# Optimization experiments

Measured on AMD Instinct MI355X. Metric: run time of the kernel, lower is better.

The kernel has to match this reference:

```python
import jax, jax.numpy as jnp
import numpy as np

B, N, D, H = 4, 2048, 512, 8
HD = D // H
SCALE = D ** (-0.5)  # module uses embed_dim**-0.5, not head_dim**-0.5


def setup_inputs() -> dict:
    key = jax.random.key(0)
    k1, k2, k3, k4 = jax.random.split(key, 4)
    x = jax.random.normal(k1, (B, N, D), dtype=jnp.float32)
    # qkv: Linear(D, 3D, bias=False); store as [D, 3D] (x @ W_qkv)
    w_qkv = jax.random.normal(k2, (D, 3 * D), dtype=jnp.float32) * (D ** -0.5)
    # out_proj: Linear(D, D) with bias
    w_out = jax.random.normal(k3, (D, D), dtype=jnp.float32) * (D ** -0.5)
    b_out = jax.random.normal(k4, (D,), dtype=jnp.float32) * 0.01
    return {"x": x, "w_qkv": w_qkv, "w_out": w_out, "b_out": b_out}


def reference(x, w_qkv, w_out, b_out):
    # qkv projection -> [B, N, 3, H, HD] -> split
    qkv = (x @ w_qkv).reshape(B, N, 3, H, HD)
    q = qkv[:, :, 0].transpose(0, 2, 1, 3)  # [B, H, N, HD]
    k = qkv[:, :, 1].transpose(0, 2, 1, 3)
    v = qkv[:, :, 2].transpose(0, 2, 1, 3)
    attn = jnp.einsum("bhqd,bhkd->bhqk", q, k) * SCALE  # [B, H, N, N]
    attn = jax.nn.softmax(attn, axis=-1)
    out = jnp.einsum("bhqk,bhkd->bhqd", attn, v)  # [B, H, N, HD]
    out = out.transpose(0, 2, 1, 3).reshape(B, N, D)
    return out @ w_out + b_out
```

## Files before the change

kernel.cpp:

```cpp
#include <hip/hip_runtime.h>

typedef __attribute__((ext_vector_type(4))) float f32x4;
typedef __attribute__((ext_vector_type(16))) float f32x16;
typedef __attribute__((ext_vector_type(8))) short short8;

#define DEV static __device__ __forceinline__

DEV unsigned short f2bf(float f) {
  union { float f; unsigned u; } x; x.f = f;
  unsigned r = x.u + 0x7fffu + ((x.u >> 16) & 1u);
  return (unsigned short)(r >> 16);
}

DEV float bf2f(unsigned short u) {
  union { unsigned u; float f; } x; x.u = ((unsigned)u) << 16;
  return x.f;
}

DEV f32x4 mfma16(short8 a, short8 b, f32x4 c) {
  return __builtin_amdgcn_mfma_f32_16x16x32_bf16(a, b, c, 0, 0, 0);
}

DEV f32x16 mfma32(short8 a, short8 b, f32x16 c) {
  return __builtin_amdgcn_mfma_f32_32x32x16_bf16(a, b, c, 0, 0, 0);
}

DEV void gload16(const void* g, void* l) {
  __builtin_amdgcn_global_load_lds(
      (const __attribute__((address_space(1))) void*)g,
      (__attribute__((address_space(3))) void*)l, 16, 0, 0);
}

DEV float exp2f_fast(float x) {
  float r;
  asm("v_exp_f32 %0, %1" : "=v"(r) : "v"(x));
  return r;
}

DEV unsigned cvtpk(float lo, float hi) {
  unsigned r;
  asm("v_cvt_pk_bf16_f32 %0, %1, %2" : "=v"(r) : "v"(lo), "v"(hi));
  return r;
}

DEV short8 mk8(unsigned w0, unsigned w1, unsigned w2, unsigned w3) {
  union { unsigned u[4]; short8 s; } x;
  x.u[0] = w0; x.u[1] = w1; x.u[2] = w2; x.u[3] = w3;
  return x.s;
}

__global__ __launch_bounds__(256) void k_convert(const float* __restrict__ in,
                                                 unsigned short* __restrict__ out) {
  size_t i = (size_t)blockIdx.x * 256 + threadIdx.x;
  const f32x4* p = (const f32x4*)(in + i * 8);
  f32x4 a = p[0], b = p[1];
  short8 r;
  r[0] = f2bf(a[0]); r[1] = f2bf(a[1]); r[2] = f2bf(a[2]); r[3] = f2bf(a[3]);
  r[4] = f2bf(b[0]); r[5] = f2bf(b[1]); r[6] = f2bf(b[2]); r[7] = f2bf(b[3]);
  *(short8*)(out + i * 8) = r;
}

__global__ __launch_bounds__(256) void k_transpose_f32_bf16(
    const float* __restrict__ in, unsigned short* __restrict__ out, int R, int C) {
  __shared__ unsigned short T[64 * 72];
  int r0 = blockIdx.y * 64, c0 = blockIdx.x * 64;
  int t = threadIdx.x;
  int rr = t >> 2, seg = t & 3;
  const float* p = in + (size_t)(r0 + rr) * C + c0 + seg * 16;
#pragma unroll
  for (int q = 0; q < 4; ++q) {
    f32x4 v = *(const f32x4*)(p + q * 4);
#pragma unroll
    for (int e = 0; e < 4; ++e) T[rr * 72 + seg * 16 + q * 4 + e] = f2bf(v[e]);
  }
  __syncthreads();
  short8 o0, o1;
#pragma unroll
  for (int e = 0; e < 8; ++e) o0[e] = (short)T[(seg * 16 + e) * 72 + rr];
#pragma unroll
  for (int e = 0; e < 8; ++e) o1[e] = (short)T[(seg * 16 + 8 + e) * 72 + rr];
  unsigned short* q2 = out + (size_t)(c0 + rr) * R + r0 + seg * 16;
  *(short8*)q2 = o0;
  *(short8*)(q2 + 8) = o1;
}

__global__ __launch_bounds__(256) void k_build_vt(const unsigned short* __restrict__ qkv,
                                                  unsigned short* __restrict__ vt) {
  __shared__ unsigned short T[64 * 72];
  int n0 = blockIdx.x * 64;
  int bh = blockIdx.y;
  int b = bh >> 3, h = bh & 7;
  int t = threadIdx.x;
  int rr = t >> 2, seg = t & 3;
  const unsigned short* p =
      qkv + (size_t)(b * 2048 + n0 + rr) * 1536 + 1024 + h * 64 + seg * 16;
  *(short8*)&T[rr * 72 + seg * 16] = *(const short8*)p;
  *(short8*)&T[rr * 72 + seg * 16 + 8] = *(const short8*)(p + 8);
  __syncthreads();
  short8 o0, o1;
#pragma unroll
  for (int e = 0; e < 8; ++e) o0[e] = (short)T[(seg * 16 + e) * 72 + rr];
#pragma unroll
  for (int e = 0; e < 8; ++e) o1[e] = (short)T[(seg * 16 + 8 + e) * 72 + rr];
  unsigned short* q2 = vt + (size_t)(bh * 64 + rr) * 2048 + n0 + seg * 16;
  *(short8*)q2 = o0;
  *(short8*)(q2 + 8) = o1;
}

template <bool F32OUT>
__global__ __launch_bounds__(256) void k_gemm_bt(
    const unsigned short* __restrict__ A, const unsigned short* __restrict__ Bt,
    void* __restrict__ Cp, const float* __restrict__ bias, int M, int N, int K) {
  __shared__ unsigned short Asm[128 * 64];
  __shared__ unsigned short Bsm[128 * 64];
  const int tid = threadIdx.x;
  const int lane = tid & 63, w = tid >> 6;
  const int wr = w >> 1, wc = w & 1;
  const int bm = blockIdx.y * 128, bn = blockIdx.x * 128;
  const int l15 = lane & 15, l4 = lane >> 4;
  f32x4 acc[4][4] = {};
  for (int k0 = 0; k0 < K; k0 += 64) {
    __syncthreads();
#pragma unroll
    for (int j = 0; j < 4; ++j) {
      int c = j * 256 + tid;
      gload16(A + (size_t)(bm + (c >> 3)) * K + k0 + ((c & 7) << 3),
              Asm + (size_t)(j * 256 + w * 64) * 8);
    }
#pragma unroll
    for (int j = 0; j < 4; ++j) {
      int c = j * 256 + tid;
      gload16(Bt + (size_t)(bn + (c >> 3)) * K + k0 + ((c & 7) << 3),
              Bsm + (size_t)(j * 256 + w * 64) * 8);
    }
    __syncthreads();
#pragma unroll
    for (int kc = 0; kc < 2; ++kc) {
      short8 av[4], bv[4];
#pragma unroll
      for (int i = 0; i < 4; ++i)
        av[i] = *(const short8*)&Asm[(wr * 64 + i * 16 + l15) * 64 + kc * 32 + l4 * 8];
#pragma unroll
      for (int j = 0; j < 4; ++j)
        bv[j] = *(const short8*)&Bsm[(wc * 64 + j * 16 + l15) * 64 + kc * 32 + l4 * 8];
#pragma unroll
      for (int i = 0; i < 4; ++i)
#pragma unroll
        for (int j = 0; j < 4; ++j)
          acc[i][j] = mfma16(av[i], bv[j], acc[i][j]);
    }
  }
#pragma unroll
  for (int i = 0; i < 4; ++i) {
#pragma unroll
    for (int j = 0; j < 4; ++j) {
      int col = bn + wc * 64 + j * 16 + l15;
      float bb = 0.f;
      if constexpr (F32OUT) bb = bias[col];
#pragma unroll
      for (int v = 0; v < 4; ++v) {
        int row = bm + wr * 64 + i * 16 + l4 * 4 + v;
        if constexpr (F32OUT) {
          ((float*)Cp)[(size_t)row * N + col] = acc[i][j][v] + bb;
        } else {
          ((unsigned short*)Cp)[(size_t)row * N + col] = f2bf(acc[i][j][v]);
        }
      }
    }
  }
}

__global__ __launch_bounds__(512, 4) void k_attn4(const unsigned short* __restrict__ qkv,
                                                  const unsigned short* __restrict__ vtg,
                                                  unsigned short* __restrict__ O) {
  __shared__ unsigned short smem[16896];
  unsigned short* Ks0 = smem;
  unsigned short* Ks1 = smem + 4096;
  unsigned short* Vs0 = smem + 8192;
  unsigned short* Vs1 = smem + 12288;
  const int tid = threadIdx.x;
  const int lane = tid & 63, w = tid >> 6;
  const int qg = w & 3, half = w >> 2;
  const int l31 = lane & 31, hi = lane >> 5;
  const int bh = blockIdx.y, b = bh >> 3, h = bh & 7;
  const int q0 = blockIdx.x * 128 + qg * 32;
  const float CL = 0.044194173824159216f * 1.4426950408889634f;

  short8 qf[4];
  {
    const unsigned short* qp = qkv + (size_t)(b * 2048 + q0 + l31) * 1536 + h * 64;
#pragma unroll
    for (int ks = 0; ks < 4; ++ks) {
      short8 raw = *(const short8*)(qp + ks * 16 + hi * 8);
      short8 f;
#pragma unroll
      for (int e = 0; e < 8; ++e)
        f[e] = (short)f2bf(bf2f((unsigned short)raw[e]) * CL);
      qf[ks] = f;
    }
  }

  const int sr = tid >> 3, seg = tid & 7;
  const unsigned short* kg = qkv + (size_t)b * 2048 * 1536 + 512 + h * 64 + seg * 8;
  const unsigned short* vg = vtg + (size_t)bh * 64 * 2048 + seg * 8;
  const int so = sr * 64 + ((seg * 8) ^ ((sr & 7) << 3));

  *(short8*)&Ks0[so] = *(const short8*)(kg + (size_t)sr * 1536);
  *(short8*)&Vs0[so] = *(const short8*)(vg + (size_t)sr * 2048);
  __syncthreads();

  const int rsw = (l31 & 7) << 3;
  const int krow = (half * 32 + l31) * 64;

  f32x16 oacc0 = {}, oacc1 = {};
  float m_run = 0.f, l_run = 0.f;
  unsigned short* kcur = Ks0; unsigned short* knxt = Ks1;
  unsigned short* vcur = Vs0; unsigned short* vnxt = Vs1;

  for (int t = 0; t < 32; ++t) {
    short8 pk, pv;
    if (t < 31) {
      int kv = (t + 1) * 64;
      pk = *(const short8*)(kg + (size_t)(kv + sr) * 1536);
      pv = *(const short8*)(vg + (size_t)sr * 2048 + kv);
    }

    f32x16 st = {};
    __builtin_amdgcn_s_setprio(1);
#pragma unroll
    for (int ks = 0; ks < 4; ++ks) {
      int col = ks * 16 + hi * 8;
      short8 kf = *(const short8*)&kcur[krow + (col ^ rsw)];
      st = mfma32(kf, qf[ks], st);
    }
    __builtin_amdgcn_s_setprio(0);

    float tm[8];
#pragma unroll
    for (int r = 0; r < 8; ++r) tm[r] = fmaxf(st[r], st[r + 8]);
    float pm = fmaxf(fmaxf(fmaxf(tm[0], tm[1]), fmaxf(tm[2], tm[3])),
                     fmaxf(fmaxf(tm[4], tm[5]), fmaxf(tm[6], tm[7])));
    pm = fmaxf(pm, __shfl_xor(pm, 32));

    if (!__all(pm <= m_run + 11.5f)) {
      float mn = fmaxf(m_run, pm);
      float al = exp2f_fast(m_run - mn);
#pragma unroll
      for (int r = 0; r < 16; ++r) {
        int qd = (r & 3) + 8 * (r >> 2) + 4 * hi;
        float a = __shfl(al, qd);
        oacc0[r] *= a;
        oacc1[r] *= a;
      }
      l_run *= al;
      m_run = mn;
    }

    float p[16];
    float la = 0.f, lb = 0.f;
#pragma unroll
    for (int r = 0; r < 8; ++r) { p[r] = exp2f_fast(st[r] - m_run); la += p[r]; }
#pragma unroll
    for (int r = 8; r < 16; ++r) { p[r] = exp2f_fast(st[r] - m_run); lb += p[r]; }
    float lsum = la + lb;
    short8 pa[2];
#pragma unroll
    for (int g = 0; g < 2; ++g) {
      unsigned pkA0 = cvtpk(p[8 * g + 0], p[8 * g + 1]);
      unsigned pkA1 = cvtpk(p[8 * g + 2], p[8 * g + 3]);
      unsigned pkB0 = cvtpk(p[8 * g + 4], p[8 * g + 5]);
      unsigned pkB1 = cvtpk(p[8 * g + 6], p[8 * g + 7]);
      unsigned tA0 = __shfl_xor(pkA0, 32), tA1 = __shfl_xor(pkA1, 32);
      unsigned tB0 = __shfl_xor(pkB0, 32), tB1 = __shfl_xor(pkB1, 32);
      unsigned w0 = hi ? tB0 : pkA0;
      unsigned w1 = hi ? tB1 : pkA1;
      unsigned w2 = hi ? pkB0 : tA0;
      unsigned w3 = hi ? pkB1 : tA1;
      pa[g] = mk8(w0, w1, w2, w3);
    }
    lsum += __shfl_xor(lsum, 32);
    l_run += lsum;

    __builtin_amdgcn_s_setprio(1);
#pragma unroll
    for (int ks = 0; ks < 2; ++ks) {
      int col = (half * 2 + ks) * 16 + hi * 8;
      short8 vf0 = *(const short8*)&vcur[l31 * 64 + (col ^ rsw)];
      short8 vf1 = *(const short8*)&vcur[(32 + l31) * 64 + (col ^ rsw)];
      oacc0 = mfma32(pa[ks], vf0, oacc0);
      oacc1 = mfma32(pa[ks], vf1, oacc1);
    }
    __builtin_amdgcn_s_setprio(0);

    if (t < 31) {
      *(short8*)&knxt[so] = pk;
      *(short8*)&vnxt[so] = pv;
    }
    __syncthreads();
    { unsigned short* tp = kcur; kcur = knxt; knxt = tp; }
    { unsigned short* tp = vcur; vcur = vnxt; vnxt = tp; }
  }

  float* Opart = (float*)smem;
  float* mlbuf = (float*)(smem + 16384);
  if (half == 1) {
    float* op = Opart + qg * 2048;
#pragma unroll
    for (int r = 0; r < 16; ++r) {
      int qd = (r & 3) + 8 * (r >> 2) + 4 * hi;
      op[qd * 64 + l31] = oacc0[r];
      op[qd * 64 + 32 + l31] = oacc1[r];
    }
    if (hi == 0) {
      mlbuf[qg * 64 + l31] = m_run;
      mlbuf[qg * 64 + 32 + l31] = l_run;
    }
  }
  __syncthreads();
  if (half == 0) {
    float mb = mlbuf[qg * 64 + l31];
    float lb2 = mlbuf[qg * 64 + 32 + l31];
    float mmax = fmaxf(m_run, mb);
    float sa = exp2f_fast(m_run - mmax);
    float sb = exp2f_fast(mb - mmax);
    float dI = 1.0f / (l_run * sa + lb2 * sb);
    float fA = sa * dI, fB = sb * dI;
    const float* op = Opart + qg * 2048;
#pragma unroll
    for (int r = 0; r < 16; ++r) {
      int qd = (r & 3) + 8 * (r >> 2) + 4 * hi;
      float fa = __shfl(fA, qd), fb = __shfl(fB, qd);
      float o0 = oacc0[r] * fa + op[qd * 64 + l31] * fb;
      float o1 = oacc1[r] * fa + op[qd * 64 + 32 + l31] * fb;
      size_t row = (size_t)(b * 2048 + q0 + qd) * 512 + h * 64;
      O[row + l31] = f2bf(o0);
      O[row + 32 + l31] = f2bf(o1);
    }
  }
}

extern "C" void kernel_launch(void* const* d_in, const int* in_sizes, int n_in,
                              void* d_out, int out_size, void* d_ws, size_t ws_size,
                              hipStream_t stream) {
  const float* x = (const float*)d_in[0];
  const float* w_qkv = (const float*)d_in[1];
  const float* w_out = (const float*)d_in[2];
  const float* b_out = (const float*)d_in[3];
  float* out = (float*)d_out;
  char* ws = (char*)d_ws;

  unsigned short* xb    = (unsigned short*)(ws + 0);
  unsigned short* wqkvT = (unsigned short*)(ws + 8388608);
  unsigned short* woutT = (unsigned short*)(ws + 9961472);
  unsigned short* qkvb  = (unsigned short*)(ws + 10485760);
  unsigned short* vtb   = (unsigned short*)(ws + 35651584);
  unsigned short* Ob    = (unsigned short*)(ws + 44040192);

  k_convert<<<2048, 256, 0, stream>>>(x, xb);
  k_transpose_f32_bf16<<<dim3(24, 8), 256, 0, stream>>>(w_qkv, wqkvT, 512, 1536);
  k_transpose_f32_bf16<<<dim3(8, 8), 256, 0, stream>>>(w_out, woutT, 512, 512);
  k_gemm_bt<false><<<dim3(12, 64), 256, 0, stream>>>(xb, wqkvT, (void*)qkvb, nullptr,
                                                     8192, 1536, 512);
  k_build_vt<<<dim3(32, 32), 256, 0, stream>>>(qkvb, vtb);
  k_attn4<<<dim3(16, 32), 512, 0, stream>>>(qkvb, vtb, Ob);
  k_gemm_bt<true><<<dim3(4, 64), 256, 0, stream>>>(Ob, woutT, (void*)out, b_out,
                                                   8192, 512, 512);
}
```

Measured before the change: 182.0 us.

## Fuse prep kernels, swizzle GEMM block order for XCDs, widen LDS XOR swizzle

Merges the x conversion and both weight transposes into one launch, removing two kernel launches. Remaps GEMM block indices so consecutive blocks are spread across the 8 XCDs, aiming for better L2 locality. Changes the attention LDS swizzle to XOR row bits 0-2 with bits 3-5, which changes the bank mapping for K and V fragment reads and may reduce conflicts. These three ideas are unrelated to one another.

```diff
diff --git a/kernel.cpp b/kernel.cpp
--- a/kernel.cpp
+++ b/kernel.cpp
@@ -49,22 +49,37 @@
   return x.s;
 }
 
-__global__ __launch_bounds__(256) void k_convert(const float* __restrict__ in,
-                                                 unsigned short* __restrict__ out) {
-  size_t i = (size_t)blockIdx.x * 256 + threadIdx.x;
-  const f32x4* p = (const f32x4*)(in + i * 8);
-  f32x4 a = p[0], b = p[1];
-  short8 r;
-  r[0] = f2bf(a[0]); r[1] = f2bf(a[1]); r[2] = f2bf(a[2]); r[3] = f2bf(a[3]);
-  r[4] = f2bf(b[0]); r[5] = f2bf(b[1]); r[6] = f2bf(b[2]); r[7] = f2bf(b[3]);
-  *(short8*)(out + i * 8) = r;
-}
-
-__global__ __launch_bounds__(256) void k_transpose_f32_bf16(
-    const float* __restrict__ in, unsigned short* __restrict__ out, int R, int C) {
+DEV int swzrow(int r) { return (((r & 7) ^ ((r >> 3) & 7)) << 3); }
+
+__global__ __launch_bounds__(256) void k_prep(
+    const float* __restrict__ x, unsigned short* __restrict__ xb,
+    const float* __restrict__ wq, unsigned short* __restrict__ wqT,
+    const float* __restrict__ wo, unsigned short* __restrict__ woT) {
   __shared__ unsigned short T[64 * 72];
-  int r0 = blockIdx.y * 64, c0 = blockIdx.x * 64;
-  int t = threadIdx.x;
+  const int blk = blockIdx.x;
+  const int t = threadIdx.x;
+  if (blk < 2048) {
+    size_t i = (size_t)blk * 256 + t;
+    const f32x4* p = (const f32x4*)(x + i * 8);
+    f32x4 a = p[0], b = p[1];
+    short8 r;
+    r[0] = f2bf(a[0]); r[1] = f2bf(a[1]); r[2] = f2bf(a[2]); r[3] = f2bf(a[3]);
+    r[4] = f2bf(b[0]); r[5] = f2bf(b[1]); r[6] = f2bf(b[2]); r[7] = f2bf(b[3]);
+    *(short8*)(xb + i * 8) = r;
+    return;
+  }
+  const float* in;
+  unsigned short* out;
+  int C, bx, by;
+  const int R = 512;
+  if (blk < 2240) {
+    in = wq; out = wqT; C = 1536;
+    int bb = blk - 2048; bx = bb % 24; by = bb / 24;
+  } else {
+    in = wo; out = woT; C = 512;
+    int bb = blk - 2240; bx = bb & 7; by = bb >> 3;
+  }
+  int r0 = by * 64, c0 = bx * 64;
   int rr = t >> 2, seg = t & 3;
   const float* p = in + (size_t)(r0 + rr) * C + c0 + seg * 16;
 #pragma unroll
@@ -116,7 +131,11 @@
   const int tid = threadIdx.x;
   const int lane = tid & 63, w = tid >> 6;
   const int wr = w >> 1, wc = w & 1;
-  const int bm = blockIdx.y * 128, bn = blockIdx.x * 128;
+  const int nbx = gridDim.x;
+  const int cpx = (nbx * gridDim.y) >> 3;
+  const int lin = blockIdx.y * nbx + blockIdx.x;
+  const int swz = (lin & 7) * cpx + (lin >> 3);
+  const int bm = (swz / nbx) * 128, bn = (swz % nbx) * 128;
   const int l15 = lane & 15, l4 = lane >> 4;
   f32x4 acc[4][4] = {};
   for (int k0 = 0; k0 < K; k0 += 64) {
@@ -170,7 +189,7 @@
   }
 }
 
-__global__ __launch_bounds__(512, 4) void k_attn4(const unsigned short* __restrict__ qkv,
+__global__ __launch_bounds__(512, 4) void k_attn5(const unsigned short* __restrict__ qkv,
                                                   const unsigned short* __restrict__ vtg,
                                                   unsigned short* __restrict__ O) {
   __shared__ unsigned short smem[16896];
@@ -203,13 +222,15 @@
   const int sr = tid >> 3, seg = tid & 7;
   const unsigned short* kg = qkv + (size_t)b * 2048 * 1536 + 512 + h * 64 + seg * 8;
   const unsigned short* vg = vtg + (size_t)bh * 64 * 2048 + seg * 8;
-  const int so = sr * 64 + ((seg * 8) ^ ((sr & 7) << 3));
+  const int so = sr * 64 + ((seg * 8) ^ swzrow(sr));
 
   *(short8*)&Ks0[so] = *(const short8*)(kg + (size_t)sr * 1536);
   *(short8*)&Vs0[so] = *(const short8*)(vg + (size_t)sr * 2048);
   __syncthreads();
 
-  const int rsw = (l31 & 7) << 3;
+  const int kxor = swzrow(half * 32 + l31);
+  const int v0xor = swzrow(l31);
+  const int v1xor = swzrow(32 + l31);
   const int krow = (half * 32 + l31) * 64;
 
   f32x16 oacc0 = {}, oacc1 = {};
@@ -230,7 +251,7 @@
 #pragma unroll
     for (int ks = 0; ks < 4; ++ks) {
       int col = ks * 16 + hi * 8;
-      short8 kf = *(const short8*)&kcur[krow + (col ^ rsw)];
+      short8 kf = *(const short8*)&kcur[krow + (col ^ kxor)];
       st = mfma32(kf, qf[ks], st);
     }
     __builtin_amdgcn_s_setprio(0);
@@ -285,8 +306,8 @@
 #pragma unroll
     for (int ks = 0; ks < 2; ++ks) {
       int col = (half * 2 + ks) * 16 + hi * 8;
-      short8 vf0 = *(const short8*)&vcur[l31 * 64 + (col ^ rsw)];
-      short8 vf1 = *(const short8*)&vcur[(32 + l31) * 64 + (col ^ rsw)];
+      short8 vf0 = *(const short8*)&vcur[l31 * 64 + (col ^ v0xor)];
+      short8 vf1 = *(const short8*)&vcur[(32 + l31) * 64 + (col ^ v1xor)];
       oacc0 = mfma32(pa[ks], vf0, oacc0);
       oacc1 = mfma32(pa[ks], vf1, oacc1);
     }
@@ -356,13 +377,11 @@
   unsigned short* vtb   = (unsigned short*)(ws + 35651584);
   unsigned short* Ob    = (unsigned short*)(ws + 44040192);
 
-  k_convert<<<2048, 256, 0, stream>>>(x, xb);
-  k_transpose_f32_bf16<<<dim3(24, 8), 256, 0, stream>>>(w_qkv, wqkvT, 512, 1536);
-  k_transpose_f32_bf16<<<dim3(8, 8), 256, 0, stream>>>(w_out, woutT, 512, 512);
+  k_prep<<<2304, 256, 0, stream>>>(x, xb, w_qkv, wqkvT, w_out, woutT);
   k_gemm_bt<false><<<dim3(12, 64), 256, 0, stream>>>(xb, wqkvT, (void*)qkvb, nullptr,
                                                      8192, 1536, 512);
   k_build_vt<<<dim3(32, 32), 256, 0, stream>>>(qkvb, vtb);
-  k_attn4<<<dim3(16, 32), 512, 0, stream>>>(qkvb, vtb, Ob);
+  k_attn5<<<dim3(16, 32), 512, 0, stream>>>(qkvb, vtb, Ob);
   k_gemm_bt<true><<<dim3(4, 64), 256, 0, stream>>>(Ob, woutT, (void*)out, b_out,
                                                    8192, 512, 512);
 }
```

New measurement: 175.4 us. -3.6%, faster.
